# Performance work log

Measured on AMD Instinct MI355X. Metric: run time of the kernel, lower is better.

## Reference

```python
import jax, jax.numpy as jnp
import numpy as np

H_HEADS = 16
D_K = 64
D_V = 64
D_MODEL = H_HEADS * D_K  # 1024
B, S = 2, 2048


def _xavier(key, shape):
    fan_in, fan_out = shape
    limit = float(np.sqrt(6.0 / (fan_in + fan_out)))
    return jax.random.uniform(key, shape, jnp.float32, -limit, limit)


def setup_inputs() -> dict:
    key = jax.random.key(0)
    ks = jax.random.split(key, 6)
    return {
        "batch": jax.random.normal(ks[0], (B, S, D_MODEL), jnp.float32),
        "attention_mask": jnp.zeros((S, S), jnp.float32),
        "W_Q": _xavier(ks[1], (D_MODEL, H_HEADS * D_K)),
        "W_K": _xavier(ks[2], (D_MODEL, H_HEADS * D_K)),
        "W_V": _xavier(ks[3], (D_MODEL, H_HEADS * D_V)),
        "b_Q": jnp.zeros((H_HEADS * D_K,), jnp.float32),
        "b_K": jnp.zeros((H_HEADS * D_K,), jnp.float32),
        "b_V": jnp.zeros((H_HEADS * D_V,), jnp.float32),
        "W_O": _xavier(ks[4], (H_HEADS * D_V, D_MODEL)),
        "b_O": jnp.zeros((D_MODEL,), jnp.float32),
    }


def reference(batch, attention_mask, W_Q, W_K, W_V, b_Q, b_K, b_V, W_O, b_O):
    # Batched equivalent of the per-head loop: project all heads at once,
    # then split the last dim into (h, d). Same math, one GEMM each.
    q = batch @ W_Q + b_Q  # [B,S,h*dk]
    k = batch @ W_K + b_K
    v = batch @ W_V + b_V
    q = q.reshape(B, S, H_HEADS, D_K)
    k = k.reshape(B, S, H_HEADS, D_K)
    v = v.reshape(B, S, H_HEADS, D_V)
    scale = 1.0 / jnp.sqrt(jnp.asarray(D_K, jnp.float32))
    scores = jnp.einsum("bqhd,bkhd->bhqk", q, k) * scale  # [B,h,S,S]
    scores = scores + attention_mask  # broadcast over batch & heads
    attn = jax.nn.softmax(scores, axis=-1)
    out = jnp.einsum("bhqk,bkhd->bqhd", attn, v)  # [B,S,h,dv]
    out = out.reshape(B, S, H_HEADS * D_V)  # concat over heads
    return out @ W_O + b_O
```

## Files before the change

kernel.cpp:

```cpp
#include <hip/hip_runtime.h>
#include <hip/hip_bf16.h>

typedef __attribute__((ext_vector_type(8))) short bf16x8;
typedef __attribute__((ext_vector_type(4))) float f32x4;
typedef __attribute__((ext_vector_type(4))) unsigned short u16x4;
typedef __attribute__((ext_vector_type(8))) unsigned short u16x8;

#define DEVI static __device__ __forceinline__

DEVI unsigned short f2bf(float f) {
  union { __hip_bfloat16 h; unsigned short u; } cv;
  cv.h = __float2bfloat16(f);
  return cv.u;
}

DEVI void gld_lds16(const unsigned short* g, unsigned short* l) {
  __builtin_amdgcn_global_load_lds(
      (const __attribute__((address_space(1))) unsigned int*)g,
      (__attribute__((address_space(3))) unsigned int*)l, 16, 0, 0);
}


__global__ void k_cvt_x(const float* __restrict__ x, unsigned short* __restrict__ xb) {
  int i = blockIdx.x * 256 + threadIdx.x;
  f32x4 v = *((const f32x4*)x + i);
  u16x4 o;
#pragma unroll
  for (int j = 0; j < 4; ++j) o[j] = f2bf(v[j]);
  *((u16x4*)xb + i) = o;
}

__global__ void k_wt(const float* __restrict__ Wq, const float* __restrict__ Wk,
                     const float* __restrict__ Wv, const float* __restrict__ Wo,
                     unsigned short* __restrict__ wqkvT, unsigned short* __restrict__ woT) {
  __shared__ float lt[32][33];
  int t = blockIdx.x;
  int g = t >> 10, r = t & 1023, kt = r >> 5, nt = r & 31;
  const float* W = (g == 0) ? Wq : (g == 1) ? Wk : (g == 2) ? Wv : Wo;
  unsigned short* out = (g < 3) ? (wqkvT + (size_t)g * 1024 * 1024) : woT;
  int tid = threadIdx.x;
  int row = tid >> 3, c4 = tid & 7;
  f32x4 v = *(const f32x4*)(W + (size_t)(kt * 32 + row) * 1024 + nt * 32 + c4 * 4);
#pragma unroll
  for (int j = 0; j < 4; ++j) lt[row][c4 * 4 + j] = v[j];
  __syncthreads();
  u16x4 o;
#pragma unroll
  for (int j = 0; j < 4; ++j) o[j] = f2bf(lt[c4 * 4 + j][row]);
  *(u16x4*)(out + (size_t)(nt * 32 + row) * 1024 + kt * 32 + c4 * 4) = o;
}

__global__ void k_bias(const float* __restrict__ bq, const float* __restrict__ bk,
                       const float* __restrict__ bv, float* __restrict__ bcat) {
  int i = blockIdx.x * 256 + threadIdx.x;
  if (i < 3072) bcat[i] = (i < 1024) ? bq[i] : (i < 2048) ? bk[i - 1024] : bv[i - 2048];
}

__global__ void k_vt(const unsigned short* __restrict__ qkv, unsigned short* __restrict__ vt) {
  __shared__ unsigned short lt[64][72];
  int bh = blockIdx.y, s0 = blockIdx.x * 64;
  int b = bh >> 4, h = bh & 15;
  int tid = threadIdx.x;
#pragma unroll
  for (int i = 0; i < 2; ++i) {
    int c = tid + i * 256;
    int row = c >> 3, c8 = (c & 7) * 8;
    u16x8 v = *(const u16x8*)(qkv + (size_t)(b * 2048 + s0 + row) * 3072 + 2048 + h * 64 + c8);
#pragma unroll
    for (int j = 0; j < 8; ++j) lt[row][c8 + j] = v[j];
  }
  __syncthreads();
#pragma unroll
  for (int i = 0; i < 2; ++i) {
    int c = tid + i * 256;
    int d = c >> 3, s8 = (c & 7) * 8;
    u16x8 o;
#pragma unroll
    for (int j = 0; j < 8; ++j) o[j] = lt[s8 + j][d];
    *(u16x8*)(vt + (size_t)(bh * 64 + d) * 2048 + s0 + s8) = o;
  }
}

template <int OUT_BF16>
__launch_bounds__(256)
__global__ void k_gemm(const unsigned short* __restrict__ A,
                       const unsigned short* __restrict__ Bt,
                       const float* __restrict__ bias, void* __restrict__ C,
                       int M, int N, int K) {
  __shared__ unsigned short lA[128 * 32];
  __shared__ unsigned short lB[128 * 32];
  int tid = threadIdx.x;
  int m0 = blockIdx.y * 128, n0 = blockIdx.x * 128;
  int w = tid >> 6, l = tid & 63;
  int wm = (w >> 1) * 64, wn = (w & 1) * 64;
  int lg = l >> 4, lc = l & 15;
  f32x4 acc[4][4] = {};
  const unsigned short* Ab = A + (size_t)m0 * K;
  const unsigned short* Bb = Bt + (size_t)n0 * K;

  for (int kk = 0; kk < K; kk += 32) {
#pragma unroll
    for (int i = 0; i < 2; ++i) {
      int c = tid + i * 256;
      int row = c >> 2, c8 = (c & 3) * 8;
      gld_lds16(Ab + (size_t)row * K + kk + c8, lA + c * 8);
    }
#pragma unroll
    for (int i = 0; i < 2; ++i) {
      int c = tid + i * 256;
      int row = c >> 2, c8 = (c & 3) * 8;
      gld_lds16(Bb + (size_t)row * K + kk + c8, lB + c * 8);
    }
    __syncthreads();
    bf16x8 af[4], bfr[4];
#pragma unroll
    for (int mf = 0; mf < 4; ++mf)
      af[mf] = *(const bf16x8*)(lA + (wm + mf * 16 + lc) * 32 + lg * 8);
#pragma unroll
    for (int nf = 0; nf < 4; ++nf)
      bfr[nf] = *(const bf16x8*)(lB + (wn + nf * 16 + lc) * 32 + lg * 8);
#pragma unroll
    for (int mf = 0; mf < 4; ++mf)
#pragma unroll
      for (int nf = 0; nf < 4; ++nf)
        acc[mf][nf] = __builtin_amdgcn_mfma_f32_16x16x32_bf16(af[mf], bfr[nf], acc[mf][nf], 0, 0, 0);
    __syncthreads();
  }

  int lr = lg * 4;
  float bv[4];
#pragma unroll
  for (int nf = 0; nf < 4; ++nf) bv[nf] = bias[n0 + wn + nf * 16 + lc];
#pragma unroll
  for (int mf = 0; mf < 4; ++mf)
#pragma unroll
    for (int nf = 0; nf < 4; ++nf)
#pragma unroll
      for (int rr = 0; rr < 4; ++rr) {
        size_t gm = m0 + wm + mf * 16 + lr + rr;
        size_t gn = n0 + wn + nf * 16 + lc;
        float v = acc[mf][nf][rr] + bv[nf];
        if (OUT_BF16)
          ((unsigned short*)C)[gm * N + gn] = f2bf(v);
        else
          ((float*)C)[gm * N + gn] = v;
      }
}

__launch_bounds__(256, 4)
__global__ void k_attn(const unsigned short* __restrict__ qkv,
                       const unsigned short* __restrict__ vt,
                       const float* __restrict__ mask,
                       unsigned short* __restrict__ ao) {
  __shared__ unsigned short lK[2][64 * 64];
  __shared__ unsigned short lV[2][64 * 64];
  __shared__ unsigned short lP[64 * 64];
  int wg = blockIdx.x;
  int b = wg >> 9, r0 = wg & 511, h = r0 >> 5, qt = r0 & 31;
  int tid = threadIdx.x, w = tid >> 6, l = tid & 63;
  int lg = l >> 4, lc = l & 15;
  int q0 = qt * 64 + w * 16;

  const unsigned short* Qb = qkv + (size_t)(b * 2048 + q0) * 3072 + h * 64;
  const unsigned short* Kb = qkv + (size_t)(b * 2048) * 3072 + 1024 + h * 64;
  const unsigned short* Vb = vt + (size_t)((b * 16 + h) * 64) * 2048;

  int rsub = l >> 3;
  int scol = ((l & 7) ^ rsub) * 8;

  bf16x8 qf[2];
#pragma unroll
  for (int ks = 0; ks < 2; ++ks)
    qf[ks] = *(const bf16x8*)(Qb + (size_t)lc * 3072 + ks * 32 + lg * 8);

  const float* mrow[4];
#pragma unroll
  for (int rr = 0; rr < 4; ++rr)
    mrow[rr] = mask + (size_t)(q0 + lg * 4 + rr) * 2048 + lc;

  f32x4 o[4] = {};
  float m[4], ll[4];
#pragma unroll
  for (int rr = 0; rr < 4; ++rr) { m[rr] = -1e30f; ll[rr] = 0.f; }

#pragma unroll
  for (int i = 0; i < 2; ++i) {
    int r = i * 32 + w * 8 + rsub;
    gld_lds16(Kb + (size_t)r * 3072 + scol, &lK[0][(i * 4 + w) * 512]);
    gld_lds16(Vb + (size_t)r * 2048 + scol, &lV[0][(i * 4 + w) * 512]);
  }
  __syncthreads();

  int cur = 0;
  for (int t = 0; t < 32; ++t) {
    int k0 = t * 64;
    if (t < 31) {
#pragma unroll
      for (int i = 0; i < 2; ++i) {
        int r = i * 32 + w * 8 + rsub;
        gld_lds16(Kb + (size_t)(k0 + 64 + r) * 3072 + scol, &lK[cur ^ 1][(i * 4 + w) * 512]);
        gld_lds16(Vb + (size_t)r * 2048 + k0 + 64 + scol, &lV[cur ^ 1][(i * 4 + w) * 512]);
      }
    }
    const unsigned short* lKc = lK[cur];
    const unsigned short* lVc = lV[cur];

    f32x4 s[4] = {};
#pragma unroll
    for (int ks = 0; ks < 2; ++ks) {
      bf16x8 kf[4];
#pragma unroll
      for (int nf = 0; nf < 4; ++nf)
        kf[nf] = *(const bf16x8*)(lKc + (nf * 16 + lc) * 64 +
                                  ((ks * 32 + lg * 8) ^ ((lc & 7) << 3)));
#pragma unroll
      for (int nf = 0; nf < 4; ++nf)
        s[nf] = __builtin_amdgcn_mfma_f32_16x16x32_bf16(qf[ks], kf[nf], s[nf], 0, 0, 0);
    }

    float sv[4][4];
#pragma unroll
    for (int nf = 0; nf < 4; ++nf)
#pragma unroll
      for (int rr = 0; rr < 4; ++rr)
        sv[nf][rr] = s[nf][rr] * 0.125f + mrow[rr][k0 + nf * 16];

    float al[4], mn[4];
#pragma unroll
    for (int rr = 0; rr < 4; ++rr) {
      float t2 = fmaxf(fmaxf(sv[0][rr], sv[1][rr]), fmaxf(sv[2][rr], sv[3][rr]));
      t2 = fmaxf(t2, __shfl_xor(t2, 1));
      t2 = fmaxf(t2, __shfl_xor(t2, 2));
      t2 = fmaxf(t2, __shfl_xor(t2, 4));
      t2 = fmaxf(t2, __shfl_xor(t2, 8));
      mn[rr] = fmaxf(m[rr], t2);
      al[rr] = __expf(m[rr] - mn[rr]);
      m[rr] = mn[rr];
    }
    float ps[4] = {0.f, 0.f, 0.f, 0.f};
#pragma unroll
    for (int nf = 0; nf < 4; ++nf)
#pragma unroll
      for (int rr = 0; rr < 4; ++rr) {
        float p = __expf(sv[nf][rr] - mn[rr]);
        ps[rr] += p;
        int prow = w * 16 + lg * 4 + rr;
        lP[prow * 64 + ((nf * 16 + lc) ^ ((prow & 7) << 3))] = f2bf(p);
      }
#pragma unroll
    for (int rr = 0; rr < 4; ++rr) {
      float t2 = ps[rr];
      t2 += __shfl_xor(t2, 1);
      t2 += __shfl_xor(t2, 2);
      t2 += __shfl_xor(t2, 4);
      t2 += __shfl_xor(t2, 8);
      ll[rr] = ll[rr] * al[rr] + t2;
    }
#pragma unroll
    for (int nf = 0; nf < 4; ++nf)
#pragma unroll
      for (int rr = 0; rr < 4; ++rr) o[nf][rr] *= al[rr];

#pragma unroll
    for (int ks2 = 0; ks2 < 2; ++ks2) {
      bf16x8 pa = *(const bf16x8*)(lP + (w * 16 + lc) * 64 +
                                   ((ks2 * 32 + lg * 8) ^ ((lc & 7) << 3)));
      bf16x8 vf[4];
#pragma unroll
      for (int nf = 0; nf < 4; ++nf)
        vf[nf] = *(const bf16x8*)(lVc + (nf * 16 + lc) * 64 +
                                  ((ks2 * 32 + lg * 8) ^ ((lc & 7) << 3)));
#pragma unroll
      for (int nf = 0; nf < 4; ++nf)
        o[nf] = __builtin_amdgcn_mfma_f32_16x16x32_bf16(pa, vf[nf], o[nf], 0, 0, 0);
    }

    __syncthreads();
    cur ^= 1;
  }

#pragma unroll
  for (int rr = 0; rr < 4; ++rr) {
    float inv = 1.f / ll[rr];
    int q = q0 + lg * 4 + rr;
#pragma unroll
    for (int nf = 0; nf < 4; ++nf)
      ao[(size_t)(b * 2048 + q) * 1024 + h * 64 + nf * 16 + lc] = f2bf(o[nf][rr] * inv);
  }
}

extern "C" void kernel_launch(void* const* d_in, const int* in_sizes, int n_in,
                              void* d_out, int out_size, void* d_ws, size_t ws_size,
                              hipStream_t stream) {
  const float* batch = (const float*)d_in[0];
  const float* mask = (const float*)d_in[1];
  const float* Wq = (const float*)d_in[2];
  const float* Wk = (const float*)d_in[3];
  const float* Wv = (const float*)d_in[4];
  const float* bq = (const float*)d_in[5];
  const float* bk = (const float*)d_in[6];
  const float* bvv = (const float*)d_in[7];
  const float* Wo = (const float*)d_in[8];
  const float* bo = (const float*)d_in[9];

  char* ws = (char*)d_ws;
  unsigned short* Xb    = (unsigned short*)(ws);
  unsigned short* WqkvT = (unsigned short*)(ws + 8388608);
  unsigned short* WoT   = (unsigned short*)(ws + 14680064);
  float*          bcat  = (float*)(ws + 16777216);
  unsigned short* QKV   = (unsigned short*)(ws + 16789504);
  unsigned short* Vt    = (unsigned short*)(ws + 41955328);
  unsigned short* AO    = (unsigned short*)(ws + 50343936);

  hipLaunchKernelGGL(k_cvt_x, dim3(4096), dim3(256), 0, stream, batch, Xb);
  hipLaunchKernelGGL(k_wt, dim3(4096), dim3(256), 0, stream, Wq, Wk, Wv, Wo, WqkvT, WoT);
  hipLaunchKernelGGL(k_bias, dim3(12), dim3(256), 0, stream, bq, bk, bvv, bcat);
  hipLaunchKernelGGL((k_gemm<1>), dim3(24, 32), dim3(256), 0, stream,
                     Xb, WqkvT, bcat, (void*)QKV, 4096, 3072, 1024);
  hipLaunchKernelGGL(k_vt, dim3(32, 32), dim3(256), 0, stream, QKV, Vt);
  hipLaunchKernelGGL(k_attn, dim3(1024), dim3(256), 0, stream, QKV, Vt, mask, AO);
  hipLaunchKernelGGL((k_gemm<0>), dim3(8, 32), dim3(256), 0, stream,
                     AO, WoT, bo, (void*)d_out, 4096, 1024, 1024);
}
```

Measured before the change: 279.8 us.

## Transpose attention MFMA so each lane owns one query row, bf16 log2 mask

Swaps the MFMA operand order in attention so each lane holds scores for a single query row across 16 keys. This replaces most cross-lane shuffle reductions for max and sum with in-register reductions and a single running max/sum per lane. A new pre-pass converts the mask to a transposed bf16 layout pre-scaled by log2(e), so the kernel uses exp2 and fma and loads mask values as packed vectors. The attention grid is remapped across XCDs, and the output goes through LDS for vectorized stores. The costs are an extra kernel launch and mask rounding to bf16.

```diff
diff --git a/kernel.cpp b/kernel.cpp
--- a/kernel.cpp
+++ b/kernel.cpp
@@ -12,6 +12,12 @@
   union { __hip_bfloat16 h; unsigned short u; } cv;
   cv.h = __float2bfloat16(f);
   return cv.u;
+}
+
+DEVI float bf2f(unsigned short u) {
+  union { unsigned int i; float f; } cv;
+  cv.i = (unsigned int)u << 16;
+  return cv.f;
 }
 
 DEVI void gld_lds16(const unsigned short* g, unsigned short* l) {
@@ -54,6 +60,22 @@
                        const float* __restrict__ bv, float* __restrict__ bcat) {
   int i = blockIdx.x * 256 + threadIdx.x;
   if (i < 3072) bcat[i] = (i < 1024) ? bq[i] : (i < 2048) ? bk[i - 1024] : bv[i - 2048];
+}
+
+__global__ void k_mt(const float* __restrict__ mask, unsigned short* __restrict__ mU) {
+  __shared__ float lt[32][33];
+  int q0 = blockIdx.y * 32, k0 = blockIdx.x * 32;
+  int tid = threadIdx.x;
+  int row = tid >> 3, c4 = tid & 7;
+  f32x4 v = *(const f32x4*)(mask + (size_t)(q0 + row) * 2048 + k0 + c4 * 4);
+#pragma unroll
+  for (int j = 0; j < 4; ++j) lt[row][c4 * 4 + j] = v[j] * 1.4426950408889634f;
+  __syncthreads();
+  int kq = tid >> 5, qr = tid & 31;
+  u16x4 o;
+#pragma unroll
+  for (int j = 0; j < 4; ++j) o[j] = f2bf(lt[qr][kq * 4 + j]);
+  *(u16x4*)(mU + ((size_t)(k0 >> 2) + kq) * 8192 + (size_t)(q0 + qr) * 4) = o;
 }
 
 __global__ void k_vt(const unsigned short* __restrict__ qkv, unsigned short* __restrict__ vt) {
@@ -150,20 +172,23 @@
 __launch_bounds__(256, 4)
 __global__ void k_attn(const unsigned short* __restrict__ qkv,
                        const unsigned short* __restrict__ vt,
-                       const float* __restrict__ mask,
+                       const unsigned short* __restrict__ mU,
                        unsigned short* __restrict__ ao) {
   __shared__ unsigned short lK[2][64 * 64];
   __shared__ unsigned short lV[2][64 * 64];
   __shared__ unsigned short lP[64 * 64];
-  int wg = blockIdx.x;
+  int wg0 = blockIdx.x;
+  int wg = (wg0 & 7) * 128 + (wg0 >> 3);
   int b = wg >> 9, r0 = wg & 511, h = r0 >> 5, qt = r0 & 31;
   int tid = threadIdx.x, w = tid >> 6, l = tid & 63;
   int lg = l >> 4, lc = l & 15;
+  int c = lc & 7;
   int q0 = qt * 64 + w * 16;
 
   const unsigned short* Qb = qkv + (size_t)(b * 2048 + q0) * 3072 + h * 64;
   const unsigned short* Kb = qkv + (size_t)(b * 2048) * 3072 + 1024 + h * 64;
   const unsigned short* Vb = vt + (size_t)((b * 16 + h) * 64) * 2048;
+  const unsigned short* mUb = mU + (size_t)lg * 8192 + (size_t)(q0 + lc) * 4;
 
   int rsub = l >> 3;
   int scol = ((l & 7) ^ rsub) * 8;
@@ -173,15 +198,8 @@
   for (int ks = 0; ks < 2; ++ks)
     qf[ks] = *(const bf16x8*)(Qb + (size_t)lc * 3072 + ks * 32 + lg * 8);
 
-  const float* mrow[4];
-#pragma unroll
-  for (int rr = 0; rr < 4; ++rr)
-    mrow[rr] = mask + (size_t)(q0 + lg * 4 + rr) * 2048 + lc;
-
-  f32x4 o[4] = {};
-  float m[4], ll[4];
-#pragma unroll
-  for (int rr = 0; rr < 4; ++rr) { m[rr] = -1e30f; ll[rr] = 0.f; }
+  f32x4 o2[4] = {};
+  float m = -1e30f, ll = 0.f;
 
 #pragma unroll
   for (int i = 0; i < 2; ++i) {
@@ -192,6 +210,7 @@
   __syncthreads();
 
   int cur = 0;
+  unsigned short* lPw = lP + (w * 16 + lc) * 64;
   for (int t = 0; t < 32; ++t) {
     int k0 = t * 64;
     if (t < 31) {
@@ -210,82 +229,86 @@
     for (int ks = 0; ks < 2; ++ks) {
       bf16x8 kf[4];
 #pragma unroll
-      for (int nf = 0; nf < 4; ++nf)
-        kf[nf] = *(const bf16x8*)(lKc + (nf * 16 + lc) * 64 +
-                                  ((ks * 32 + lg * 8) ^ ((lc & 7) << 3)));
-#pragma unroll
-      for (int nf = 0; nf < 4; ++nf)
-        s[nf] = __builtin_amdgcn_mfma_f32_16x16x32_bf16(qf[ks], kf[nf], s[nf], 0, 0, 0);
-    }
-
-    float sv[4][4];
+      for (int blk = 0; blk < 4; ++blk)
+        kf[blk] = *(const bf16x8*)(lKc + (blk * 16 + lc) * 64 +
+                                   ((ks * 32 + lg * 8) ^ (c << 3)));
+#pragma unroll
+      for (int blk = 0; blk < 4; ++blk)
+        s[blk] = __builtin_amdgcn_mfma_f32_16x16x32_bf16(kf[blk], qf[ks], s[blk], 0, 0, 0);
+    }
+
+    float tl[16];
+#pragma unroll
+    for (int blk = 0; blk < 4; ++blk) {
+      u16x4 mv = *(const u16x4*)(mUb + ((size_t)(k0 >> 2) + blk * 4) * 8192);
+#pragma unroll
+      for (int rr = 0; rr < 4; ++rr)
+        tl[blk * 4 + rr] = fmaf(s[blk][rr], 0.18033688011112042f, bf2f(mv[rr]));
+    }
+
+    float tm[8];
+#pragma unroll
+    for (int i = 0; i < 8; ++i) tm[i] = fmaxf(tl[2 * i], tl[2 * i + 1]);
+#pragma unroll
+    for (int i = 0; i < 4; ++i) tm[i] = fmaxf(tm[2 * i], tm[2 * i + 1]);
+    float mx = fmaxf(fmaxf(tm[0], tm[1]), fmaxf(tm[2], tm[3]));
+    mx = fmaxf(mx, __shfl_xor(mx, 16));
+    mx = fmaxf(mx, __shfl_xor(mx, 32));
+    float mn = fmaxf(m, mx);
+    float al = exp2f(m - mn);
+    m = mn;
+
+    float psum = 0.f;
+#pragma unroll
+    for (int blk = 0; blk < 4; ++blk) {
+      u16x4 pk;
+#pragma unroll
+      for (int rr = 0; rr < 4; ++rr) {
+        float p = exp2f(tl[blk * 4 + rr] - mn);
+        psum += p;
+        pk[rr] = f2bf(p);
+      }
+      *(u16x4*)(lPw + (((blk * 32 + lg * 8) ^ (c << 4)) >> 1)) = pk;
+    }
+    ll = ll * al + psum;
 #pragma unroll
     for (int nf = 0; nf < 4; ++nf)
 #pragma unroll
-      for (int rr = 0; rr < 4; ++rr)
-        sv[nf][rr] = s[nf][rr] * 0.125f + mrow[rr][k0 + nf * 16];
-
-    float al[4], mn[4];
-#pragma unroll
-    for (int rr = 0; rr < 4; ++rr) {
-      float t2 = fmaxf(fmaxf(sv[0][rr], sv[1][rr]), fmaxf(sv[2][rr], sv[3][rr]));
-      t2 = fmaxf(t2, __shfl_xor(t2, 1));
-      t2 = fmaxf(t2, __shfl_xor(t2, 2));
-      t2 = fmaxf(t2, __shfl_xor(t2, 4));
-      t2 = fmaxf(t2, __shfl_xor(t2, 8));
-      mn[rr] = fmaxf(m[rr], t2);
-      al[rr] = __expf(m[rr] - mn[rr]);
-      m[rr] = mn[rr];
-    }
-    float ps[4] = {0.f, 0.f, 0.f, 0.f};
-#pragma unroll
-    for (int nf = 0; nf < 4; ++nf)
-#pragma unroll
-      for (int rr = 0; rr < 4; ++rr) {
-        float p = __expf(sv[nf][rr] - mn[rr]);
-        ps[rr] += p;
-        int prow = w * 16 + lg * 4 + rr;
-        lP[prow * 64 + ((nf * 16 + lc) ^ ((prow & 7) << 3))] = f2bf(p);
-      }
-#pragma unroll
-    for (int rr = 0; rr < 4; ++rr) {
-      float t2 = ps[rr];
-      t2 += __shfl_xor(t2, 1);
-      t2 += __shfl_xor(t2, 2);
-      t2 += __shfl_xor(t2, 4);
-      t2 += __shfl_xor(t2, 8);
-      ll[rr] = ll[rr] * al[rr] + t2;
-    }
-#pragma unroll
-    for (int nf = 0; nf < 4; ++nf)
-#pragma unroll
-      for (int rr = 0; rr < 4; ++rr) o[nf][rr] *= al[rr];
+      for (int rr = 0; rr < 4; ++rr) o2[nf][rr] *= al;
 
 #pragma unroll
     for (int ks2 = 0; ks2 < 2; ++ks2) {
-      bf16x8 pa = *(const bf16x8*)(lP + (w * 16 + lc) * 64 +
-                                   ((ks2 * 32 + lg * 8) ^ ((lc & 7) << 3)));
+      bf16x8 pa = *(const bf16x8*)(lPw + (((ks2 * 64 + lg * 16) ^ (c << 4)) >> 1));
       bf16x8 vf[4];
 #pragma unroll
       for (int nf = 0; nf < 4; ++nf)
         vf[nf] = *(const bf16x8*)(lVc + (nf * 16 + lc) * 64 +
-                                  ((ks2 * 32 + lg * 8) ^ ((lc & 7) << 3)));
+                                  ((ks2 * 32 + lg * 8) ^ (c << 3)));
 #pragma unroll
       for (int nf = 0; nf < 4; ++nf)
-        o[nf] = __builtin_amdgcn_mfma_f32_16x16x32_bf16(pa, vf[nf], o[nf], 0, 0, 0);
+        o2[nf] = __builtin_amdgcn_mfma_f32_16x16x32_bf16(vf[nf], pa, o2[nf], 0, 0, 0);
     }
 
     __syncthreads();
     cur ^= 1;
   }
 
-#pragma unroll
-  for (int rr = 0; rr < 4; ++rr) {
-    float inv = 1.f / ll[rr];
-    int q = q0 + lg * 4 + rr;
-#pragma unroll
-    for (int nf = 0; nf < 4; ++nf)
-      ao[(size_t)(b * 2048 + q) * 1024 + h * 64 + nf * 16 + lc] = f2bf(o[nf][rr] * inv);
+  ll += __shfl_xor(ll, 16);
+  ll += __shfl_xor(ll, 32);
+  float inv = 1.f / ll;
+#pragma unroll
+  for (int nf = 0; nf < 4; ++nf) {
+    u16x4 pk;
+#pragma unroll
+    for (int rr = 0; rr < 4; ++rr) pk[rr] = f2bf(o2[nf][rr] * inv);
+    *(u16x4*)(lPw + (((nf * 32 + lg * 8) ^ (c << 4)) >> 1)) = pk;
+  }
+  int rq = l >> 2, seg = l & 3, c2 = rq & 7;
+  const unsigned short* lPr = lP + (w * 16 + rq) * 64;
+#pragma unroll
+  for (int half = 0; half < 2; ++half) {
+    u16x8 ov = *(const u16x8*)(lPr + (((seg * 32 + half * 16) ^ (c2 << 4)) >> 1));
+    *(u16x8*)(ao + (size_t)(b * 2048 + q0 + rq) * 1024 + h * 64 + seg * 16 + half * 8) = ov;
   }
 }
 
@@ -311,14 +334,16 @@
   unsigned short* QKV   = (unsigned short*)(ws + 16789504);
   unsigned short* Vt    = (unsigned short*)(ws + 41955328);
   unsigned short* AO    = (unsigned short*)(ws + 50343936);
+  unsigned short* mU    = Xb;
 
   hipLaunchKernelGGL(k_cvt_x, dim3(4096), dim3(256), 0, stream, batch, Xb);
   hipLaunchKernelGGL(k_wt, dim3(4096), dim3(256), 0, stream, Wq, Wk, Wv, Wo, WqkvT, WoT);
   hipLaunchKernelGGL(k_bias, dim3(12), dim3(256), 0, stream, bq, bk, bvv, bcat);
   hipLaunchKernelGGL((k_gemm<1>), dim3(24, 32), dim3(256), 0, stream,
                      Xb, WqkvT, bcat, (void*)QKV, 4096, 3072, 1024);
+  hipLaunchKernelGGL(k_mt, dim3(64, 64), dim3(256), 0, stream, mask, mU);
   hipLaunchKernelGGL(k_vt, dim3(32, 32), dim3(256), 0, stream, QKV, Vt);
-  hipLaunchKernelGGL(k_attn, dim3(1024), dim3(256), 0, stream, QKV, Vt, mask, AO);
+  hipLaunchKernelGGL(k_attn, dim3(1024), dim3(256), 0, stream, QKV, Vt, mU, AO);
   hipLaunchKernelGGL((k_gemm<0>), dim3(8, 32), dim3(256), 0, stream,
                      AO, WoT, bo, (void*)d_out, 4096, 1024, 1024);
 }
```

After: 260.0 us. -7.1%, faster.
